# Performance work log

Hardware: AMD Instinct MI355X
Metric: run time of the kernel (lower is better)

The kernel has to match this reference:

```python
import jax, jax.numpy as jnp
import numpy as np

N_NODES = 50000
N_EDGES = 800000
F_IN = 64
F_HID = 64
F_OUT = 16


def setup_inputs() -> dict:
    key = jax.random.key(0)
    k1, k2, k3, k4, k5 = jax.random.split(key, 5)
    x = jax.random.normal(k1, (N_NODES, F_IN), dtype=jnp.float32)
    edge_index = jax.random.randint(k2, (2, N_EDGES), 0, N_NODES, dtype=jnp.int64)
    # glorot-style init for GCNConv weights
    W1 = jax.random.normal(k3, (F_IN, F_HID), dtype=jnp.float32) * (1.0 / np.sqrt(F_IN))
    b1 = jnp.zeros((F_HID,), dtype=jnp.float32)
    W2 = jax.random.normal(k4, (F_HID, F_OUT), dtype=jnp.float32) * (1.0 / np.sqrt(F_HID))
    b2 = jnp.zeros((F_OUT,), dtype=jnp.float32)
    return {"x": x, "edge_index": edge_index, "W1": W1, "b1": b1, "W2": W2, "b2": b2}


def _gcn_conv(x, src, dst, n, W, b):
    # linear transform first (PyG GCNConv), then normalized scatter-add aggregation
    h = x @ W  # [N, F_out]
    deg = jax.ops.segment_sum(jnp.ones_like(dst, dtype=h.dtype), dst, num_segments=n)
    dinv = jnp.where(deg > 0, jax.lax.rsqrt(deg), 0.0)  # deg^{-1/2}, 0 for isolated
    norm = dinv[src] * dinv[dst]  # [E]
    out = jax.ops.segment_sum(norm[:, None] * h[src], dst, num_segments=n)
    return out + b


def reference(x, edge_index, W1, b1, W2, b2):
    n = x.shape[0]
    loops = jnp.arange(n, dtype=edge_index.dtype)
    # add self-loops as in PyG GCNConv default
    src = jnp.concatenate([edge_index[0], loops])
    dst = jnp.concatenate([edge_index[1], loops])
    h = jax.nn.relu(_gcn_conv(x, src, dst, n, W1, b1))
    h = _gcn_conv(h, src, dst, n, W2, b2)
    return jax.nn.log_softmax(h, axis=1)
```

## Files before the change

### kernel.cpp

```cpp
#include <hip/hip_runtime.h>


#define F1 64
#define F2 16
#define G 256
#define HP 256

typedef __attribute__((ext_vector_type(8))) short bf16x8;
typedef __attribute__((ext_vector_type(4))) float f32x4;
typedef __attribute__((ext_vector_type(4))) unsigned short u16x4;

__device__ inline unsigned short f2bf(float f) {
    unsigned u = __float_as_uint(f);
    return (unsigned short)((u + 0x7FFFu + ((u >> 16) & 1u)) >> 16);
}
__device__ inline float bf2f(unsigned short s) {
    return __uint_as_float(((unsigned)s) << 16);
}

__device__ inline void cvt8(const float* v, bf16x8& h, bf16x8& l) {
#pragma unroll
    for (int i = 0; i < 8; ++i) {
        unsigned b = __float_as_uint(v[i]);
        h[i] = (short)(b >> 16);
        float hif = __uint_as_float(b & 0xFFFF0000u);
        float lof = v[i] - hif;
        l[i] = (short)(__float_as_uint(lof) >> 16);
    }
}


__global__ __launch_bounds__(256) void k_hist(const int4* __restrict__ dst4,
                                              const int* __restrict__ dst,
                                              int* __restrict__ hist, int e4, int e) {
    __shared__ int hl[HP];
    int tid = threadIdx.x, g = blockIdx.x;
    hl[tid] = 0;
    __syncthreads();
    int chunk = (e4 + G - 1) / G;
    int beg = g * chunk, end = min(e4, beg + chunk);
    for (int i = beg + tid; i < end; i += 256) {
        int4 d = dst4[i];
        atomicAdd(&hl[d.x >> 8], 1);
        atomicAdd(&hl[d.y >> 8], 1);
        atomicAdd(&hl[d.z >> 8], 1);
        atomicAdd(&hl[d.w >> 8], 1);
    }
    if (g == G - 1)
        for (int i = e4 * 4 + tid; i < e; i += 256) atomicAdd(&hl[dst[i] >> 8], 1);
    __syncthreads();
    hist[g * HP + tid] = hl[tid];
}

__global__ __launch_bounds__(256) void k_cscan(const int* __restrict__ hist,
                                               int* __restrict__ pgoff,
                                               int* __restrict__ ptotal) {
    __shared__ int s[G];
    int p = blockIdx.x, g = threadIdx.x;
    int v = hist[g * HP + p];
    s[g] = v;
    __syncthreads();
    for (int off = 1; off < G; off <<= 1) {
        int t = (g >= off) ? s[g - off] : 0;
        __syncthreads();
        s[g] += t;
        __syncthreads();
    }
    pgoff[g * HP + p] = s[g] - v;
    if (g == G - 1) ptotal[p] = s[g];
}

__global__ __launch_bounds__(256) void k_pm1(const float* __restrict__ x,
                                             const float* __restrict__ W1,
                                             unsigned short* __restrict__ h_bf,
                                             const int4* __restrict__ src4,
                                             const int4* __restrict__ dst4,
                                             const int* __restrict__ src,
                                             const int* __restrict__ dst,
                                             const int* __restrict__ pgoff,
                                             const int* __restrict__ ptotal,
                                             unsigned* __restrict__ pairs,
                                             int e4, int e, int npart,
                                             int n, int nb1) {
    __shared__ float ws[64 * 65];
    __shared__ int s[HP], cur[HP];
    int tid = threadIdx.x;
    if ((int)blockIdx.x < nb1) {
        for (int i = tid; i < 64 * 64; i += 256) {
            int k = i >> 6, c = i & 63;
            ws[k * 65 + c] = W1[i];
        }
        __syncthreads();
        int lane = tid & 63, wv = tid >> 6;
        int rt = blockIdx.x * 64 + wv * 16;
        int r = lane & 15, g = lane >> 4;
        int row = rt + r;
        int rowc = row < n ? row : n - 1;
        const float* xp = x + (size_t)rowc * F1 + g * 8;
        bf16x8 ah[2], al[2];
#pragma unroll
        for (int kb = 0; kb < 2; ++kb) {
            float v[8];
            *(float4*)&v[0] = *(const float4*)(xp + kb * 32);
            *(float4*)&v[4] = *(const float4*)(xp + kb * 32 + 4);
            cvt8(v, ah[kb], al[kb]);
        }
#pragma unroll
        for (int ct = 0; ct < 4; ++ct) {
            bf16x8 bh[2], bl[2];
#pragma unroll
            for (int kb = 0; kb < 2; ++kb) {
                float v[8];
#pragma unroll
                for (int i = 0; i < 8; ++i)
                    v[i] = ws[(kb * 32 + g * 8 + i) * 65 + ct * 16 + r];
                cvt8(v, bh[kb], bl[kb]);
            }
            f32x4 acc = {0.f, 0.f, 0.f, 0.f};
#pragma unroll
            for (int kb = 0; kb < 2; ++kb) {
                acc = __builtin_amdgcn_mfma_f32_16x16x32_bf16(ah[kb], bh[kb], acc, 0, 0, 0);
                acc = __builtin_amdgcn_mfma_f32_16x16x32_bf16(al[kb], bh[kb], acc, 0, 0, 0);
                acc = __builtin_amdgcn_mfma_f32_16x16x32_bf16(ah[kb], bl[kb], acc, 0, 0, 0);
            }
#pragma unroll
            for (int j = 0; j < 4; ++j) {
                int orow = rt + g * 4 + j;
                if (orow < n) h_bf[(size_t)orow * F1 + ct * 16 + r] = f2bf(acc[j]);
            }
        }
    } else {
        int g = blockIdx.x - nb1;
        int v = (tid < npart) ? ptotal[tid] : 0;
        s[tid] = v;
        __syncthreads();
        for (int off = 1; off < HP; off <<= 1) {
            int t = (tid >= off) ? s[tid - off] : 0;
            __syncthreads();
            s[tid] += t;
            __syncthreads();
        }
        cur[tid] = (s[tid] - v) + pgoff[g * HP + tid];
        __syncthreads();
        int chunk = (e4 + G - 1) / G;
        int beg = g * chunk, end = min(e4, beg + chunk);
        for (int i = beg + tid; i < end; i += 256) {
            int4 s4 = src4[i];
            int4 d4 = dst4[i];
            int pos;
            pos = atomicAdd(&cur[d4.x >> 8], 1); pairs[pos] = ((unsigned)(d4.x & 255) << 16) | (unsigned)s4.x;
            pos = atomicAdd(&cur[d4.y >> 8], 1); pairs[pos] = ((unsigned)(d4.y & 255) << 16) | (unsigned)s4.y;
            pos = atomicAdd(&cur[d4.z >> 8], 1); pairs[pos] = ((unsigned)(d4.z & 255) << 16) | (unsigned)s4.z;
            pos = atomicAdd(&cur[d4.w >> 8], 1); pairs[pos] = ((unsigned)(d4.w & 255) << 16) | (unsigned)s4.w;
        }
        if (g == G - 1)
            for (int i = e4 * 4 + tid; i < e; i += 256) {
                int d = dst[i];
                int pos = atomicAdd(&cur[d >> 8], 1);
                pairs[pos] = ((unsigned)(d & 255) << 16) | (unsigned)src[i];
            }
    }
}

__global__ __launch_bounds__(256) void k_csr(const unsigned* __restrict__ pairs,
                                             const int* __restrict__ ptotal,
                                             int* __restrict__ rowstart,
                                             float* __restrict__ dinv,
                                             int* __restrict__ csr,
                                             int n, int e, int npart) {
    __shared__ int s[HP];
    __shared__ int cnt[256], cur[256];
    __shared__ int wbs, wes;
    int p = blockIdx.x, tid = threadIdx.x;
    int v = (tid < npart) ? ptotal[tid] : 0;
    s[tid] = v;
    __syncthreads();
    for (int off = 1; off < HP; off <<= 1) {
        int t = (tid >= off) ? s[tid - off] : 0;
        __syncthreads();
        s[tid] += t;
        __syncthreads();
    }
    if (tid == p) { wbs = s[tid] - v; wes = s[tid]; }
    cnt[tid] = 0;
    __syncthreads();
    int wbeg = wbs, wend = wes;
    for (int i = wbeg + tid; i < wend; i += 256)
        atomicAdd(&cnt[pairs[i] >> 16], 1);
    __syncthreads();
    int c = cnt[tid];
    s[tid] = c;
    __syncthreads();
    for (int off = 1; off < 256; off <<= 1) {
        int t = (tid >= off) ? s[tid - off] : 0;
        __syncthreads();
        s[tid] += t;
        __syncthreads();
    }
    int rs = wbeg + s[tid] - c;
    cur[tid] = rs;
    int node = (p << 8) + tid;
    if (node < n) {
        rowstart[node] = rs;
        dinv[node] = rsqrtf((float)c + 1.0f);
    }
    if (p == 0 && tid == 0) rowstart[n] = e;
    __syncthreads();
    for (int i = wbeg + tid; i < wend; i += 256) {
        unsigned u = pairs[i];
        int pos = atomicAdd(&cur[u >> 16], 1);
        csr[pos] = (int)(u & 0xFFFFu);
    }
}

__global__ __launch_bounds__(256) void k_mgemm2(const unsigned short* __restrict__ a1b,
                                                const float* __restrict__ W2,
                                                unsigned short* __restrict__ h2_bf, int n) {
    __shared__ float ws[64 * 17];
    int tid = threadIdx.x;
    for (int i = tid; i < 64 * 16; i += 256) {
        int k = i >> 4, c = i & 15;
        ws[k * 17 + c] = W2[i];
    }
    __syncthreads();
    int lane = tid & 63, wv = tid >> 6;
    int rt = blockIdx.x * 64 + wv * 16;
    int r = lane & 15, g = lane >> 4;
    int row = rt + r;
    int rowc = row < n ? row : n - 1;
    const unsigned short* ap = a1b + (size_t)rowc * F1 + g * 8;
    bf16x8 ah[2];
    ah[0] = *(const bf16x8*)(ap);
    ah[1] = *(const bf16x8*)(ap + 32);
    bf16x8 bh[2], bl[2];
#pragma unroll
    for (int kb = 0; kb < 2; ++kb) {
        float v[8];
#pragma unroll
        for (int i = 0; i < 8; ++i)
            v[i] = ws[(kb * 32 + g * 8 + i) * 17 + r];
        cvt8(v, bh[kb], bl[kb]);
    }
    f32x4 acc = {0.f, 0.f, 0.f, 0.f};
#pragma unroll
    for (int kb = 0; kb < 2; ++kb) {
        acc = __builtin_amdgcn_mfma_f32_16x16x32_bf16(ah[kb], bh[kb], acc, 0, 0, 0);
        acc = __builtin_amdgcn_mfma_f32_16x16x32_bf16(ah[kb], bl[kb], acc, 0, 0, 0);
    }
#pragma unroll
    for (int j = 0; j < 4; ++j) {
        int orow = rt + g * 4 + j;
        if (orow < n) h2_bf[(size_t)orow * F2 + r] = f2bf(acc[j]);
    }
}


__global__ __launch_bounds__(256) void k_agg64(const int* __restrict__ rowstart,
                                               const int* __restrict__ csr,
                                               const float* __restrict__ dinv,
                                               const unsigned short* __restrict__ hb,
                                               const float* __restrict__ b1,
                                               unsigned short* __restrict__ a1b, int n) {
    int lane = threadIdx.x & 63, wv = threadIdx.x >> 6;
    int node = blockIdx.x * 4 + wv;
    if (node >= n) return;
    int g = lane >> 4, q = lane & 15;
    float di = dinv[node];
    float4 acc = {0.f, 0.f, 0.f, 0.f};
    int beg = rowstart[node], end = rowstart[node + 1];
    for (int base = beg; base < end; base += 64) {
        int k = base + lane;
        int idx = (k < end) ? csr[k] : 0;
        float dv = (k < end) ? dinv[idx] : 0.0f;
        int m = end - base;
        if (m <= 32) {
#pragma unroll
            for (int i = 0; i < 8; ++i) {
                int slot = i * 4 + g;
                int s = __shfl(idx, slot, 64);
                float w = __shfl(dv, slot, 64);
                u16x4 u = *(const u16x4*)(hb + (size_t)s * F1 + q * 4);
                acc.x = fmaf(w, bf2f(u.x), acc.x);
                acc.y = fmaf(w, bf2f(u.y), acc.y);
                acc.z = fmaf(w, bf2f(u.z), acc.z);
                acc.w = fmaf(w, bf2f(u.w), acc.w);
            }
        } else {
#pragma unroll
            for (int i = 0; i < 16; ++i) {
                int slot = i * 4 + g;
                int s = __shfl(idx, slot, 64);
                float w = __shfl(dv, slot, 64);
                u16x4 u = *(const u16x4*)(hb + (size_t)s * F1 + q * 4);
                acc.x = fmaf(w, bf2f(u.x), acc.x);
                acc.y = fmaf(w, bf2f(u.y), acc.y);
                acc.z = fmaf(w, bf2f(u.z), acc.z);
                acc.w = fmaf(w, bf2f(u.w), acc.w);
            }
        }
    }
#pragma unroll
    for (int off = 16; off <= 32; off <<= 1) {
        acc.x += __shfl_xor(acc.x, off, 64);
        acc.y += __shfl_xor(acc.y, off, 64);
        acc.z += __shfl_xor(acc.z, off, 64);
        acc.w += __shfl_xor(acc.w, off, 64);
    }
    if (g == 0) {
        u16x4 su = *(const u16x4*)(hb + (size_t)node * F1 + q * 4);
        float4 bv = ((const float4*)b1)[q];
        float d2 = di * di;
        float4 o;
        o.x = fmaxf(fmaf(di, acc.x, fmaf(d2, bf2f(su.x), bv.x)), 0.f);
        o.y = fmaxf(fmaf(di, acc.y, fmaf(d2, bf2f(su.y), bv.y)), 0.f);
        o.z = fmaxf(fmaf(di, acc.z, fmaf(d2, bf2f(su.z), bv.z)), 0.f);
        o.w = fmaxf(fmaf(di, acc.w, fmaf(d2, bf2f(su.w), bv.w)), 0.f);
        u16x4 rv;
        rv.x = f2bf(o.x); rv.y = f2bf(o.y); rv.z = f2bf(o.z); rv.w = f2bf(o.w);
        *(u16x4*)(a1b + (size_t)node * F1 + q * 4) = rv;
    }
}

__global__ __launch_bounds__(256) void k_agg16(const int* __restrict__ rowstart,
                                               const int* __restrict__ csr,
                                               const float* __restrict__ dinv,
                                               const unsigned short* __restrict__ h2b,
                                               const float* __restrict__ b2,
                                               float* __restrict__ out, int n) {
    int lane = threadIdx.x & 63, wv = threadIdx.x >> 6;
    int node = blockIdx.x * 4 + wv;
    if (node >= n) return;
    int g = lane >> 2, q = lane & 3;
    float di = dinv[node];
    float4 acc = {0.f, 0.f, 0.f, 0.f};
    int beg = rowstart[node], end = rowstart[node + 1];
    for (int base = beg; base < end; base += 64) {
        int k = base + lane;
        int idx = (k < end) ? csr[k] : 0;
        float dv = (k < end) ? dinv[idx] : 0.0f;
#pragma unroll
        for (int i = 0; i < 4; ++i) {
            int slot = i * 16 + g;
            int s = __shfl(idx, slot, 64);
            float w = __shfl(dv, slot, 64);
            u16x4 u = *(const u16x4*)(h2b + (size_t)s * F2 + q * 4);
            acc.x = fmaf(w, bf2f(u.x), acc.x);
            acc.y = fmaf(w, bf2f(u.y), acc.y);
            acc.z = fmaf(w, bf2f(u.z), acc.z);
            acc.w = fmaf(w, bf2f(u.w), acc.w);
        }
    }
#pragma unroll
    for (int off = 4; off <= 32; off <<= 1) {
        acc.x += __shfl_xor(acc.x, off, 64);
        acc.y += __shfl_xor(acc.y, off, 64);
        acc.z += __shfl_xor(acc.z, off, 64);
        acc.w += __shfl_xor(acc.w, off, 64);
    }
    u16x4 su = *(const u16x4*)(h2b + (size_t)node * F2 + q * 4);
    float4 bv = ((const float4*)b2)[q];
    float d2 = di * di;
    float4 v;
    v.x = fmaf(di, acc.x, fmaf(d2, bf2f(su.x), bv.x));
    v.y = fmaf(di, acc.y, fmaf(d2, bf2f(su.y), bv.y));
    v.z = fmaf(di, acc.z, fmaf(d2, bf2f(su.z), bv.z));
    v.w = fmaf(di, acc.w, fmaf(d2, bf2f(su.w), bv.w));
    float mr = fmaxf(fmaxf(v.x, v.y), fmaxf(v.z, v.w));
    mr = fmaxf(mr, __shfl_xor(mr, 1, 64));
    mr = fmaxf(mr, __shfl_xor(mr, 2, 64));
    float sm = expf(v.x - mr) + expf(v.y - mr) + expf(v.z - mr) + expf(v.w - mr);
    sm += __shfl_xor(sm, 1, 64);
    sm += __shfl_xor(sm, 2, 64);
    float l = mr + logf(sm);
    if (g == 0) {
        float4 o;
        o.x = v.x - l; o.y = v.y - l; o.z = v.z - l; o.w = v.w - l;
        ((float4*)out)[(size_t)node * 4 + q] = o;
    }
}

extern "C" void kernel_launch(void* const* d_in, const int* in_sizes, int n_in,
                              void* d_out, int out_size, void* d_ws, size_t ws_size,
                              hipStream_t stream) {
    const float* x  = (const float*)d_in[0];
    const int*   ei = (const int*)d_in[1];
    const float* W1 = (const float*)d_in[2];
    const float* b1 = (const float*)d_in[3];
    const float* W2 = (const float*)d_in[4];
    const float* b2 = (const float*)d_in[5];
    float* out = (float*)d_out;

    const int n = in_sizes[0] / F1;
    const int e = in_sizes[1] / 2;
    const int e4 = e >> 2;
    const int* src = ei;
    const int* dst = ei + e;

    const int na = (n + 63) & ~63;
    const int npart = (n + 255) >> 8;
    const int nb1 = (n + 63) / 64;

    float* dinv     = (float*)d_ws;
    int* rowstart   = (int*)(dinv + na);
    int* ptotal     = rowstart + na + 64;
    int* csr        = ptotal + 256;
    unsigned short* h_bf = (unsigned short*)(csr + ((e + 63) & ~63));
    unsigned short* a1b  = h_bf + (size_t)n * F1;
    int* hist       = (int*)(a1b + (size_t)n * F1);
    int* pgoff      = hist + G * HP;
    unsigned* pairs = (unsigned*)(pgoff + G * HP);
    unsigned short* h2_bf = h_bf;

    k_hist <<<G, 256, 0, stream>>>((const int4*)dst, dst, hist, e4, e);
    k_cscan<<<npart, 256, 0, stream>>>(hist, pgoff, ptotal);
    k_pm1  <<<nb1 + G, 256, 0, stream>>>(x, W1, h_bf,
                                         (const int4*)src, (const int4*)dst, src, dst,
                                         pgoff, ptotal, pairs, e4, e, npart, n, nb1);
    k_csr  <<<npart, 256, 0, stream>>>(pairs, ptotal, rowstart, dinv, csr, n, e, npart);

    k_agg64<<<(n + 3) / 4, 256, 0, stream>>>(rowstart, csr, dinv, h_bf, b1, a1b, n);

    k_mgemm2<<<(n + 63) / 64, 256, 0, stream>>>(a1b, W2, h2_bf, n);
    k_agg16<<<(n + 3) / 4, 256, 0, stream>>>(rowstart, csr, dinv, h2_bf, b2, out, n);
}
```

Measured before the change: 150.5 us.

## Replace CSR build with partition-local LDS atomic aggregation over bucketed pairs

Drops the per-partition CSR construction kernel and instead aggregates directly from the destination-bucketed (dst_local, src) pairs. Each 256-node partition accumulates into a shared-memory float tile with LDS atomics and then applies self-loop, bias and activation or log-softmax. Degrees are now counted with global atomics in the histogram kernel, and dinv is computed in extra blocks of the scan kernel. This removes one kernel and the CSR writes, but only ~196 blocks are launched for each aggregation pass. That means low parallelism, heavy contended LDS atomics, and a 64KB shared tile that limits occupancy.

```diff
diff --git a/kernel.cpp b/kernel.cpp
--- a/kernel.cpp
+++ b/kernel.cpp
@@ -32,7 +32,8 @@
 
 __global__ __launch_bounds__(256) void k_hist(const int4* __restrict__ dst4,
                                               const int* __restrict__ dst,
-                                              int* __restrict__ hist, int e4, int e) {
+                                              int* __restrict__ hist,
+                                              int* __restrict__ cnt, int e4, int e) {
     __shared__ int hl[HP];
     int tid = threadIdx.x, g = blockIdx.x;
     hl[tid] = 0;
@@ -45,16 +46,32 @@
         atomicAdd(&hl[d.y >> 8], 1);
         atomicAdd(&hl[d.z >> 8], 1);
         atomicAdd(&hl[d.w >> 8], 1);
+        atomicAdd(&cnt[d.x], 1);
+        atomicAdd(&cnt[d.y], 1);
+        atomicAdd(&cnt[d.z], 1);
+        atomicAdd(&cnt[d.w], 1);
     }
     if (g == G - 1)
-        for (int i = e4 * 4 + tid; i < e; i += 256) atomicAdd(&hl[dst[i] >> 8], 1);
+        for (int i = e4 * 4 + tid; i < e; i += 256) {
+            int d = dst[i];
+            atomicAdd(&hl[d >> 8], 1);
+            atomicAdd(&cnt[d], 1);
+        }
     __syncthreads();
     hist[g * HP + tid] = hl[tid];
 }
 
 __global__ __launch_bounds__(256) void k_cscan(const int* __restrict__ hist,
                                                int* __restrict__ pgoff,
-                                               int* __restrict__ ptotal) {
+                                               int* __restrict__ ptotal,
+                                               const int* __restrict__ cnt,
+                                               float* __restrict__ dinv,
+                                               int n, int npart) {
+    if ((int)blockIdx.x >= npart) {
+        int i = ((int)blockIdx.x - npart) * 256 + threadIdx.x;
+        if (i < n) dinv[i] = rsqrtf((float)cnt[i] + 1.0f);
+        return;
+    }
     __shared__ int s[G];
     int p = blockIdx.x, g = threadIdx.x;
     int v = hist[g * HP + p];
@@ -162,54 +179,115 @@
     }
 }
 
-__global__ __launch_bounds__(256) void k_csr(const unsigned* __restrict__ pairs,
-                                             const int* __restrict__ ptotal,
-                                             int* __restrict__ rowstart,
-                                             float* __restrict__ dinv,
-                                             int* __restrict__ csr,
-                                             int n, int e, int npart) {
-    __shared__ int s[HP];
-    __shared__ int cnt[256], cur[256];
+
+__global__ __launch_bounds__(512) void k_pagg64(const unsigned* __restrict__ pairs,
+                                                const int* __restrict__ ptotal,
+                                                const float* __restrict__ dinv,
+                                                const unsigned short* __restrict__ hb,
+                                                const float* __restrict__ b1,
+                                                unsigned short* __restrict__ a1b,
+                                                int n, int npart) {
+    __shared__ __align__(16) float facc[256 * F1];
+    __shared__ int swin[HP];
+    __shared__ float sdinv[256];
     __shared__ int wbs, wes;
     int p = blockIdx.x, tid = threadIdx.x;
-    int v = (tid < npart) ? ptotal[tid] : 0;
-    s[tid] = v;
+    int v = (tid < HP && tid < npart) ? ptotal[tid] : 0;
+    if (tid < HP) swin[tid] = v;
     __syncthreads();
     for (int off = 1; off < HP; off <<= 1) {
-        int t = (tid >= off) ? s[tid - off] : 0;
-        __syncthreads();
-        s[tid] += t;
-        __syncthreads();
-    }
-    if (tid == p) { wbs = s[tid] - v; wes = s[tid]; }
-    cnt[tid] = 0;
+        int t = (tid >= off && tid < HP) ? swin[tid - off] : 0;
+        __syncthreads();
+        if (tid < HP) swin[tid] += t;
+        __syncthreads();
+    }
+    if (tid == p) { wbs = swin[tid] - v; wes = swin[tid]; }
+    if (tid < 256) {
+        int node = (p << 8) + tid;
+        sdinv[tid] = (node < n) ? dinv[node] : 0.f;
+    }
+    for (int i = tid; i < 256 * (F1 / 4); i += 512)
+        ((float4*)facc)[i] = make_float4(0.f, 0.f, 0.f, 0.f);
     __syncthreads();
     int wbeg = wbs, wend = wes;
-    for (int i = wbeg + tid; i < wend; i += 256)
-        atomicAdd(&cnt[pairs[i] >> 16], 1);
-    __syncthreads();
-    int c = cnt[tid];
-    s[tid] = c;
-    __syncthreads();
-    for (int off = 1; off < 256; off <<= 1) {
-        int t = (tid >= off) ? s[tid - off] : 0;
-        __syncthreads();
-        s[tid] += t;
-        __syncthreads();
-    }
-    int rs = wbeg + s[tid] - c;
-    cur[tid] = rs;
-    int node = (p << 8) + tid;
-    if (node < n) {
-        rowstart[node] = rs;
-        dinv[node] = rsqrtf((float)c + 1.0f);
-    }
-    if (p == 0 && tid == 0) rowstart[n] = e;
-    __syncthreads();
-    for (int i = wbeg + tid; i < wend; i += 256) {
+    int lane = tid & 63, wv = tid >> 6;
+    for (int i = wbeg + wv; i < wend; i += 8) {
         unsigned u = pairs[i];
-        int pos = atomicAdd(&cur[u >> 16], 1);
-        csr[pos] = (int)(u & 0xFFFFu);
+        int dl = u >> 16;
+        int s = (int)(u & 0xFFFFu);
+        float w = dinv[s] * sdinv[dl];
+        float hv = bf2f(hb[(size_t)s * F1 + lane]);
+        atomicAdd(&facc[dl * F1 + lane], w * hv);
+    }
+    __syncthreads();
+    float bl = b1[lane];
+    for (int nd = wv; nd < 256; nd += 8) {
+        int node = (p << 8) + nd;
+        if (node < n) {
+            float di = sdinv[nd];
+            float self = bf2f(hb[(size_t)node * F1 + lane]);
+            float o = fmaxf(fmaf(di * di, self, facc[nd * F1 + lane]) + bl, 0.f);
+            a1b[(size_t)node * F1 + lane] = f2bf(o);
+        }
+    }
+}
+
+__global__ __launch_bounds__(512) void k_pagg16(const unsigned* __restrict__ pairs,
+                                                const int* __restrict__ ptotal,
+                                                const float* __restrict__ dinv,
+                                                const unsigned short* __restrict__ h2b,
+                                                const float* __restrict__ b2,
+                                                float* __restrict__ out,
+                                                int n, int npart) {
+    __shared__ __align__(16) float facc[256 * F2];
+    __shared__ int swin[HP];
+    __shared__ float sdinv[256];
+    __shared__ int wbs, wes;
+    int p = blockIdx.x, tid = threadIdx.x;
+    int v = (tid < HP && tid < npart) ? ptotal[tid] : 0;
+    if (tid < HP) swin[tid] = v;
+    __syncthreads();
+    for (int off = 1; off < HP; off <<= 1) {
+        int t = (tid >= off && tid < HP) ? swin[tid - off] : 0;
+        __syncthreads();
+        if (tid < HP) swin[tid] += t;
+        __syncthreads();
+    }
+    if (tid == p) { wbs = swin[tid] - v; wes = swin[tid]; }
+    if (tid < 256) {
+        int node = (p << 8) + tid;
+        sdinv[tid] = (node < n) ? dinv[node] : 0.f;
+    }
+    for (int i = tid; i < 256 * (F2 / 4); i += 512)
+        ((float4*)facc)[i] = make_float4(0.f, 0.f, 0.f, 0.f);
+    __syncthreads();
+    int wbeg = wbs, wend = wes;
+    int f = tid & 15, grp = tid >> 4;
+    for (int i = wbeg + grp; i < wend; i += 32) {
+        unsigned u = pairs[i];
+        int dl = u >> 16;
+        int s = (int)(u & 0xFFFFu);
+        float w = dinv[s] * sdinv[dl];
+        float hv = bf2f(h2b[(size_t)s * F2 + f]);
+        atomicAdd(&facc[dl * F2 + f], w * hv);
+    }
+    __syncthreads();
+    float bf = b2[f];
+#pragma unroll
+    for (int pass = 0; pass < 8; ++pass) {
+        int nd = pass * 32 + grp;
+        int node = (p << 8) + nd;
+        if (node < n) {
+            float di = sdinv[nd];
+            float self = bf2f(h2b[(size_t)node * F2 + f]);
+            float vv = fmaf(di * di, self, facc[nd * F2 + f]) + bf;
+            float mr = vv;
+            for (int o = 1; o < 16; o <<= 1) mr = fmaxf(mr, __shfl_xor(mr, o, 16));
+            float ex = expf(vv - mr);
+            float sm = ex;
+            for (int o = 1; o < 16; o <<= 1) sm += __shfl_xor(sm, o, 16);
+            out[(size_t)node * F2 + f] = vv - mr - logf(sm);
+        }
     }
 }
 
@@ -254,131 +332,6 @@
     }
 }
 
-
-__global__ __launch_bounds__(256) void k_agg64(const int* __restrict__ rowstart,
-                                               const int* __restrict__ csr,
-                                               const float* __restrict__ dinv,
-                                               const unsigned short* __restrict__ hb,
-                                               const float* __restrict__ b1,
-                                               unsigned short* __restrict__ a1b, int n) {
-    int lane = threadIdx.x & 63, wv = threadIdx.x >> 6;
-    int node = blockIdx.x * 4 + wv;
-    if (node >= n) return;
-    int g = lane >> 4, q = lane & 15;
-    float di = dinv[node];
-    float4 acc = {0.f, 0.f, 0.f, 0.f};
-    int beg = rowstart[node], end = rowstart[node + 1];
-    for (int base = beg; base < end; base += 64) {
-        int k = base + lane;
-        int idx = (k < end) ? csr[k] : 0;
-        float dv = (k < end) ? dinv[idx] : 0.0f;
-        int m = end - base;
-        if (m <= 32) {
-#pragma unroll
-            for (int i = 0; i < 8; ++i) {
-                int slot = i * 4 + g;
-                int s = __shfl(idx, slot, 64);
-                float w = __shfl(dv, slot, 64);
-                u16x4 u = *(const u16x4*)(hb + (size_t)s * F1 + q * 4);
-                acc.x = fmaf(w, bf2f(u.x), acc.x);
-                acc.y = fmaf(w, bf2f(u.y), acc.y);
-                acc.z = fmaf(w, bf2f(u.z), acc.z);
-                acc.w = fmaf(w, bf2f(u.w), acc.w);
-            }
-        } else {
-#pragma unroll
-            for (int i = 0; i < 16; ++i) {
-                int slot = i * 4 + g;
-                int s = __shfl(idx, slot, 64);
-                float w = __shfl(dv, slot, 64);
-                u16x4 u = *(const u16x4*)(hb + (size_t)s * F1 + q * 4);
-                acc.x = fmaf(w, bf2f(u.x), acc.x);
-                acc.y = fmaf(w, bf2f(u.y), acc.y);
-                acc.z = fmaf(w, bf2f(u.z), acc.z);
-                acc.w = fmaf(w, bf2f(u.w), acc.w);
-            }
-        }
-    }
-#pragma unroll
-    for (int off = 16; off <= 32; off <<= 1) {
-        acc.x += __shfl_xor(acc.x, off, 64);
-        acc.y += __shfl_xor(acc.y, off, 64);
-        acc.z += __shfl_xor(acc.z, off, 64);
-        acc.w += __shfl_xor(acc.w, off, 64);
-    }
-    if (g == 0) {
-        u16x4 su = *(const u16x4*)(hb + (size_t)node * F1 + q * 4);
-        float4 bv = ((const float4*)b1)[q];
-        float d2 = di * di;
-        float4 o;
-        o.x = fmaxf(fmaf(di, acc.x, fmaf(d2, bf2f(su.x), bv.x)), 0.f);
-        o.y = fmaxf(fmaf(di, acc.y, fmaf(d2, bf2f(su.y), bv.y)), 0.f);
-        o.z = fmaxf(fmaf(di, acc.z, fmaf(d2, bf2f(su.z), bv.z)), 0.f);
-        o.w = fmaxf(fmaf(di, acc.w, fmaf(d2, bf2f(su.w), bv.w)), 0.f);
-        u16x4 rv;
-        rv.x = f2bf(o.x); rv.y = f2bf(o.y); rv.z = f2bf(o.z); rv.w = f2bf(o.w);
-        *(u16x4*)(a1b + (size_t)node * F1 + q * 4) = rv;
-    }
-}
-
-__global__ __launch_bounds__(256) void k_agg16(const int* __restrict__ rowstart,
-                                               const int* __restrict__ csr,
-                                               const float* __restrict__ dinv,
-                                               const unsigned short* __restrict__ h2b,
-                                               const float* __restrict__ b2,
-                                               float* __restrict__ out, int n) {
-    int lane = threadIdx.x & 63, wv = threadIdx.x >> 6;
-    int node = blockIdx.x * 4 + wv;
-    if (node >= n) return;
-    int g = lane >> 2, q = lane & 3;
-    float di = dinv[node];
-    float4 acc = {0.f, 0.f, 0.f, 0.f};
-    int beg = rowstart[node], end = rowstart[node + 1];
-    for (int base = beg; base < end; base += 64) {
-        int k = base + lane;
-        int idx = (k < end) ? csr[k] : 0;
-        float dv = (k < end) ? dinv[idx] : 0.0f;
-#pragma unroll
-        for (int i = 0; i < 4; ++i) {
-            int slot = i * 16 + g;
-            int s = __shfl(idx, slot, 64);
-            float w = __shfl(dv, slot, 64);
-            u16x4 u = *(const u16x4*)(h2b + (size_t)s * F2 + q * 4);
-            acc.x = fmaf(w, bf2f(u.x), acc.x);
-            acc.y = fmaf(w, bf2f(u.y), acc.y);
-            acc.z = fmaf(w, bf2f(u.z), acc.z);
-            acc.w = fmaf(w, bf2f(u.w), acc.w);
-        }
-    }
-#pragma unroll
-    for (int off = 4; off <= 32; off <<= 1) {
-        acc.x += __shfl_xor(acc.x, off, 64);
-        acc.y += __shfl_xor(acc.y, off, 64);
-        acc.z += __shfl_xor(acc.z, off, 64);
-        acc.w += __shfl_xor(acc.w, off, 64);
-    }
-    u16x4 su = *(const u16x4*)(h2b + (size_t)node * F2 + q * 4);
-    float4 bv = ((const float4*)b2)[q];
-    float d2 = di * di;
-    float4 v;
-    v.x = fmaf(di, acc.x, fmaf(d2, bf2f(su.x), bv.x));
-    v.y = fmaf(di, acc.y, fmaf(d2, bf2f(su.y), bv.y));
-    v.z = fmaf(di, acc.z, fmaf(d2, bf2f(su.z), bv.z));
-    v.w = fmaf(di, acc.w, fmaf(d2, bf2f(su.w), bv.w));
-    float mr = fmaxf(fmaxf(v.x, v.y), fmaxf(v.z, v.w));
-    mr = fmaxf(mr, __shfl_xor(mr, 1, 64));
-    mr = fmaxf(mr, __shfl_xor(mr, 2, 64));
-    float sm = expf(v.x - mr) + expf(v.y - mr) + expf(v.z - mr) + expf(v.w - mr);
-    sm += __shfl_xor(sm, 1, 64);
-    sm += __shfl_xor(sm, 2, 64);
-    float l = mr + logf(sm);
-    if (g == 0) {
-        float4 o;
-        o.x = v.x - l; o.y = v.y - l; o.z = v.z - l; o.w = v.w - l;
-        ((float4*)out)[(size_t)node * 4 + q] = o;
-    }
-}
-
 extern "C" void kernel_launch(void* const* d_in, const int* in_sizes, int n_in,
                               void* d_out, int out_size, void* d_ws, size_t ws_size,
                               hipStream_t stream) {
@@ -399,27 +352,27 @@
     const int na = (n + 63) & ~63;
     const int npart = (n + 255) >> 8;
     const int nb1 = (n + 63) / 64;
+    const int ndb = (n + 255) / 256;
 
     float* dinv     = (float*)d_ws;
-    int* rowstart   = (int*)(dinv + na);
-    int* ptotal     = rowstart + na + 64;
-    int* csr        = ptotal + 256;
-    unsigned short* h_bf = (unsigned short*)(csr + ((e + 63) & ~63));
+    int* cnt        = (int*)(dinv + na);
+    int* ptotal     = cnt + na;
+    unsigned short* h_bf = (unsigned short*)(ptotal + 256);
     unsigned short* a1b  = h_bf + (size_t)n * F1;
     int* hist       = (int*)(a1b + (size_t)n * F1);
     int* pgoff      = hist + G * HP;
     unsigned* pairs = (unsigned*)(pgoff + G * HP);
     unsigned short* h2_bf = h_bf;
 
-    k_hist <<<G, 256, 0, stream>>>((const int4*)dst, dst, hist, e4, e);
-    k_cscan<<<npart, 256, 0, stream>>>(hist, pgoff, ptotal);
+    hipMemsetAsync(cnt, 0, (size_t)n * sizeof(int), stream);
+    k_hist <<<G, 256, 0, stream>>>((const int4*)dst, dst, hist, cnt, e4, e);
+    k_cscan<<<npart + ndb, 256, 0, stream>>>(hist, pgoff, ptotal, cnt, dinv, n, npart);
     k_pm1  <<<nb1 + G, 256, 0, stream>>>(x, W1, h_bf,
                                          (const int4*)src, (const int4*)dst, src, dst,
                                          pgoff, ptotal, pairs, e4, e, npart, n, nb1);
-    k_csr  <<<npart, 256, 0, stream>>>(pairs, ptotal, rowstart, dinv, csr, n, e, npart);
-
-    k_agg64<<<(n + 3) / 4, 256, 0, stream>>>(rowstart, csr, dinv, h_bf, b1, a1b, n);
+
+    k_pagg64<<<npart, 512, 0, stream>>>(pairs, ptotal, dinv, h_bf, b1, a1b, n, npart);
 
     k_mgemm2<<<(n + 63) / 64, 256, 0, stream>>>(a1b, W2, h2_bf, n);
-    k_agg16<<<(n + 3) / 4, 256, 0, stream>>>(rowstart, csr, dinv, h2_bf, b2, out, n);
-}
+    k_pagg16<<<npart, 512, 0, stream>>>(pairs, ptotal, dinv, h2_bf, b2, out, n, npart);
+}
```

Result: slower. 581.4 us (+286.3%).

## Fuse second-layer linear transform into first aggregation, use 16-bit CSR indices

Applied to the files above, without the earlier changes.

The first-layer aggregation epilogue now applies bias and ReLU, then multiplies by W2 in registers, holding 4x4 slices of W2 per lane. Lanes reduce the partial products with shuffles and write the 16-wide bf16 h2 directly. This removes the separate MFMA GEMM kernel and the 64-wide intermediate activation write and reread. CSR column indices are also stored as 16-bit values, halving index traffic in both aggregation kernels. That relies on node counts below 65536, which the packed pair format already assumed.

```diff
diff --git a/kernel.cpp b/kernel.cpp
--- a/kernel.cpp
+++ b/kernel.cpp
@@ -166,7 +166,7 @@
                                              const int* __restrict__ ptotal,
                                              int* __restrict__ rowstart,
                                              float* __restrict__ dinv,
-                                             int* __restrict__ csr,
+                                             unsigned short* __restrict__ csr,
                                              int n, int e, int npart) {
     __shared__ int s[HP];
     __shared__ int cnt[256], cur[256];
@@ -209,68 +209,36 @@
     for (int i = wbeg + tid; i < wend; i += 256) {
         unsigned u = pairs[i];
         int pos = atomicAdd(&cur[u >> 16], 1);
-        csr[pos] = (int)(u & 0xFFFFu);
-    }
-}
-
-__global__ __launch_bounds__(256) void k_mgemm2(const unsigned short* __restrict__ a1b,
-                                                const float* __restrict__ W2,
-                                                unsigned short* __restrict__ h2_bf, int n) {
-    __shared__ float ws[64 * 17];
-    int tid = threadIdx.x;
-    for (int i = tid; i < 64 * 16; i += 256) {
-        int k = i >> 4, c = i & 15;
-        ws[k * 17 + c] = W2[i];
-    }
-    __syncthreads();
-    int lane = tid & 63, wv = tid >> 6;
-    int rt = blockIdx.x * 64 + wv * 16;
-    int r = lane & 15, g = lane >> 4;
-    int row = rt + r;
-    int rowc = row < n ? row : n - 1;
-    const unsigned short* ap = a1b + (size_t)rowc * F1 + g * 8;
-    bf16x8 ah[2];
-    ah[0] = *(const bf16x8*)(ap);
-    ah[1] = *(const bf16x8*)(ap + 32);
-    bf16x8 bh[2], bl[2];
-#pragma unroll
-    for (int kb = 0; kb < 2; ++kb) {
-        float v[8];
-#pragma unroll
-        for (int i = 0; i < 8; ++i)
-            v[i] = ws[(kb * 32 + g * 8 + i) * 17 + r];
-        cvt8(v, bh[kb], bl[kb]);
-    }
-    f32x4 acc = {0.f, 0.f, 0.f, 0.f};
-#pragma unroll
-    for (int kb = 0; kb < 2; ++kb) {
-        acc = __builtin_amdgcn_mfma_f32_16x16x32_bf16(ah[kb], bh[kb], acc, 0, 0, 0);
-        acc = __builtin_amdgcn_mfma_f32_16x16x32_bf16(ah[kb], bl[kb], acc, 0, 0, 0);
-    }
-#pragma unroll
-    for (int j = 0; j < 4; ++j) {
-        int orow = rt + g * 4 + j;
-        if (orow < n) h2_bf[(size_t)orow * F2 + r] = f2bf(acc[j]);
+        csr[pos] = (unsigned short)(u & 0xFFFFu);
     }
 }
 
 
 __global__ __launch_bounds__(256) void k_agg64(const int* __restrict__ rowstart,
-                                               const int* __restrict__ csr,
+                                               const unsigned short* __restrict__ csr,
                                                const float* __restrict__ dinv,
                                                const unsigned short* __restrict__ hb,
                                                const float* __restrict__ b1,
-                                               unsigned short* __restrict__ a1b, int n) {
+                                               const float* __restrict__ W2,
+                                               unsigned short* __restrict__ h2_bf, int n) {
     int lane = threadIdx.x & 63, wv = threadIdx.x >> 6;
     int node = blockIdx.x * 4 + wv;
     if (node >= n) return;
     int g = lane >> 4, q = lane & 15;
+    float wreg[4][4], b1r[4];
+#pragma unroll
+    for (int t = 0; t < 4; ++t) {
+        b1r[t] = b1[q * 4 + t];
+#pragma unroll
+        for (int u = 0; u < 4; ++u)
+            wreg[t][u] = W2[(q * 4 + t) * F2 + g * 4 + u];
+    }
     float di = dinv[node];
     float4 acc = {0.f, 0.f, 0.f, 0.f};
     int beg = rowstart[node], end = rowstart[node + 1];
     for (int base = beg; base < end; base += 64) {
         int k = base + lane;
-        int idx = (k < end) ? csr[k] : 0;
+        int idx = (k < end) ? (int)csr[k] : 0;
         float dv = (k < end) ? dinv[idx] : 0.0f;
         int m = end - base;
         if (m <= 32) {
@@ -306,23 +274,30 @@
         acc.z += __shfl_xor(acc.z, off, 64);
         acc.w += __shfl_xor(acc.w, off, 64);
     }
-    if (g == 0) {
-        u16x4 su = *(const u16x4*)(hb + (size_t)node * F1 + q * 4);
-        float4 bv = ((const float4*)b1)[q];
-        float d2 = di * di;
-        float4 o;
-        o.x = fmaxf(fmaf(di, acc.x, fmaf(d2, bf2f(su.x), bv.x)), 0.f);
-        o.y = fmaxf(fmaf(di, acc.y, fmaf(d2, bf2f(su.y), bv.y)), 0.f);
-        o.z = fmaxf(fmaf(di, acc.z, fmaf(d2, bf2f(su.z), bv.z)), 0.f);
-        o.w = fmaxf(fmaf(di, acc.w, fmaf(d2, bf2f(su.w), bv.w)), 0.f);
+    u16x4 su = *(const u16x4*)(hb + (size_t)node * F1 + q * 4);
+    float d2 = di * di;
+    float a0 = fmaxf(fmaf(di, acc.x, fmaf(d2, bf2f(su.x), b1r[0])), 0.f);
+    float a1 = fmaxf(fmaf(di, acc.y, fmaf(d2, bf2f(su.y), b1r[1])), 0.f);
+    float a2 = fmaxf(fmaf(di, acc.z, fmaf(d2, bf2f(su.z), b1r[2])), 0.f);
+    float a3 = fmaxf(fmaf(di, acc.w, fmaf(d2, bf2f(su.w), b1r[3])), 0.f);
+    float p[4];
+#pragma unroll
+    for (int u = 0; u < 4; ++u)
+        p[u] = fmaf(a0, wreg[0][u], fmaf(a1, wreg[1][u],
+               fmaf(a2, wreg[2][u], a3 * wreg[3][u])));
+#pragma unroll
+    for (int off = 1; off <= 8; off <<= 1)
+#pragma unroll
+        for (int u = 0; u < 4; ++u) p[u] += __shfl_xor(p[u], off, 64);
+    if (q == 0) {
         u16x4 rv;
-        rv.x = f2bf(o.x); rv.y = f2bf(o.y); rv.z = f2bf(o.z); rv.w = f2bf(o.w);
-        *(u16x4*)(a1b + (size_t)node * F1 + q * 4) = rv;
+        rv.x = f2bf(p[0]); rv.y = f2bf(p[1]); rv.z = f2bf(p[2]); rv.w = f2bf(p[3]);
+        *(u16x4*)(h2_bf + (size_t)node * F2 + g * 4) = rv;
     }
 }
 
 __global__ __launch_bounds__(256) void k_agg16(const int* __restrict__ rowstart,
-                                               const int* __restrict__ csr,
+                                               const unsigned short* __restrict__ csr,
                                                const float* __restrict__ dinv,
                                                const unsigned short* __restrict__ h2b,
                                                const float* __restrict__ b2,
@@ -336,7 +311,7 @@
     int beg = rowstart[node], end = rowstart[node + 1];
     for (int base = beg; base < end; base += 64) {
         int k = base + lane;
-        int idx = (k < end) ? csr[k] : 0;
+        int idx = (k < end) ? (int)csr[k] : 0;
         float dv = (k < end) ? dinv[idx] : 0.0f;
 #pragma unroll
         for (int i = 0; i < 4; ++i) {
@@ -403,13 +378,12 @@
     float* dinv     = (float*)d_ws;
     int* rowstart   = (int*)(dinv + na);
     int* ptotal     = rowstart + na + 64;
-    int* csr        = ptotal + 256;
-    unsigned short* h_bf = (unsigned short*)(csr + ((e + 63) & ~63));
-    unsigned short* a1b  = h_bf + (size_t)n * F1;
-    int* hist       = (int*)(a1b + (size_t)n * F1);
+    unsigned short* csr = (unsigned short*)(ptotal + 256);
+    unsigned short* h_bf = csr + (((size_t)e + 63) & ~(size_t)63);
+    unsigned short* h2_bf = h_bf + (size_t)n * F1;
+    int* hist       = (int*)(h2_bf + (size_t)n * F2 + 64);
     int* pgoff      = hist + G * HP;
     unsigned* pairs = (unsigned*)(pgoff + G * HP);
-    unsigned short* h2_bf = h_bf;
 
     k_hist <<<G, 256, 0, stream>>>((const int4*)dst, dst, hist, e4, e);
     k_cscan<<<npart, 256, 0, stream>>>(hist, pgoff, ptotal);
@@ -418,8 +392,7 @@
                                          pgoff, ptotal, pairs, e4, e, npart, n, nb1);
     k_csr  <<<npart, 256, 0, stream>>>(pairs, ptotal, rowstart, dinv, csr, n, e, npart);
 
-    k_agg64<<<(n + 3) / 4, 256, 0, stream>>>(rowstart, csr, dinv, h_bf, b1, a1b, n);
-
-    k_mgemm2<<<(n + 63) / 64, 256, 0, stream>>>(a1b, W2, h2_bf, n);
+    k_agg64<<<(n + 3) / 4, 256, 0, stream>>>(rowstart, csr, dinv, h_bf, b1, W2, h2_bf, n);
+
     k_agg16<<<(n + 3) / 4, 256, 0, stream>>>(rowstart, csr, dinv, h2_bf, b2, out, n);
 }
```

After: 171.6 us. 14.0% more time.
